# Performance work log

Hardware: AMD Instinct MI355X
Metric: run time of the kernel (lower is better)

The kernel has to match this reference:

```python
import jax, jax.numpy as jnp
import numpy as np

N_NODES = 100000
N_EDGES = 1600000
IN_DIM = 128
HID = 128


def sage_conv(x, src, dst, W_l, W_r, b, num_nodes):
    # PyG SAGEConv (mean aggregation): out = lin_l(mean_{j in N(i)} x_j) + lin_r(x_i)
    msgs = x[src]                                            # [E, F] gather
    agg = jax.ops.segment_sum(msgs, dst, num_segments=num_nodes)  # [N, F]
    cnt = jax.ops.segment_sum(jnp.ones((src.shape[0],), x.dtype), dst,
                              num_segments=num_nodes)        # [N]
    agg = agg / jnp.maximum(cnt, 1.0)[:, None]               # mean; 0 for isolated nodes
    return agg @ W_l + b + x @ W_r


def setup_inputs() -> dict:
    key = jax.random.key(0)
    ks = jax.random.split(key, 12)
    s_in = 1.0 / np.sqrt(IN_DIM)
    s_h = 1.0 / np.sqrt(HID)
    return {
        "x": jax.random.normal(ks[0], (N_NODES, IN_DIM), jnp.float32),
        "edge_index": jax.random.randint(ks[1], (2, N_EDGES), 0, N_NODES, jnp.int64),
        "Wl1": jax.random.normal(ks[2], (IN_DIM, HID), jnp.float32) * s_in,
        "Wr1": jax.random.normal(ks[3], (IN_DIM, HID), jnp.float32) * s_in,
        "b1": jnp.zeros((HID,), jnp.float32),
        "Wl2": jax.random.normal(ks[4], (HID, HID), jnp.float32) * s_h,
        "Wr2": jax.random.normal(ks[5], (HID, HID), jnp.float32) * s_h,
        "b2": jnp.zeros((HID,), jnp.float32),
        "Wp": jax.random.normal(ks[6], (HID, 1), jnp.float32) * s_h,
        "bp": jnp.zeros((1,), jnp.float32),
        "Wd": jax.random.normal(ks[7], (HID, 1), jnp.float32) * s_h,
        "bd": jnp.zeros((1,), jnp.float32),
    }


def reference(x, edge_index, Wl1, Wr1, b1, Wl2, Wr2, b2, Wp, bp, Wd, bd):
    src, dst = edge_index[0], edge_index[1]
    h = jax.nn.relu(sage_conv(x, src, dst, Wl1, Wr1, b1, N_NODES))
    h = jax.nn.relu(sage_conv(h, src, dst, Wl2, Wr2, b2, N_NODES))
    preds = h @ Wp + bp                      # [N, 1]
    diffs = jax.nn.sigmoid(h @ Wd + bd)      # [N, 1]
    return (preds - diffs, preds + diffs)
```

## Files before the change

### kernel.cpp

```cpp
#include <hip/hip_runtime.h>
#include <hip/hip_bf16.h>

#define N_NODES 100000
#define N_EDGES 1600000
#define NBUCK 1563
#define BCAP 1216
#define PADC 1408
#define ACHUNK 4096
#define GTILES 1563
#define PABLK 391

typedef __bf16 bf16x8 __attribute__((ext_vector_type(8)));
typedef __bf16 bf16x4 __attribute__((ext_vector_type(4)));
typedef float  f32x4  __attribute__((ext_vector_type(4)));
typedef float  f32x2  __attribute__((ext_vector_type(2)));


#define ACC16(v)                                             \
  a01 += __builtin_amdgcn_cvt_pk_f32_fp8((v).x, false);      \
  a23 += __builtin_amdgcn_cvt_pk_f32_fp8((v).x, true);       \
  a45 += __builtin_amdgcn_cvt_pk_f32_fp8((v).y, false);      \
  a67 += __builtin_amdgcn_cvt_pk_f32_fp8((v).y, true);       \
  a89 += __builtin_amdgcn_cvt_pk_f32_fp8((v).z, false);      \
  aAB += __builtin_amdgcn_cvt_pk_f32_fp8((v).z, true);       \
  aCD += __builtin_amdgcn_cvt_pk_f32_fp8((v).w, false);      \
  aEF += __builtin_amdgcn_cvt_pk_f32_fp8((v).w, true);

#define WFRAG(ct, c) (*(const bf16x8*)&Wswz[(size_t)((((w * 4 + (ct)) * 4 + (c)) * 64) + lane) * 8])


__global__ __launch_bounds__(256) void init_kernel(int* __restrict__ bcnt,
                                                   int* __restrict__ P1s,
                                                   int* __restrict__ P2s,
                                                   const float* __restrict__ Wl1,
                                                   const float* __restrict__ Wr1,
                                                   const float* __restrict__ Wl2,
                                                   const float* __restrict__ Wr2,
                                                   __bf16* __restrict__ W1out,
                                                   __bf16* __restrict__ W2out) {
  const int b = blockIdx.x, t = threadIdx.x;
  if (b == 0) {
    for (int i = t; i < NBUCK; i += 256) bcnt[i] = 0;
    if (t < 32) { P1s[t] = 0; P2s[t] = 0; }
    return;
  }
  int gi = (b - 1) * 256 + t;
  bool L2 = gi >= 32768;
  int i = gi & 32767;
  int j = i & 7;
  int lane = (i >> 3) & 63;
  int c = (i >> 9) & 3;
  int tile = i >> 11;
  int k = c * 32 + ((lane >> 4) * 8) + j;
  int krow = L2 ? (((k & 7) << 4) | (k >> 3)) : k;
  int col = tile * 16 + (lane & 15);
  const float* Wl = L2 ? Wl2 : Wl1;
  const float* Wr = L2 ? Wr2 : Wr1;
  float v = (col < 128) ? Wl[krow * 128 + col] : Wr[krow * 128 + (col - 128)];
  (L2 ? W2out : W1out)[i] = (__bf16)v;
}


__global__ __launch_bounds__(256, 4) void work1_kernel(
    const float* __restrict__ A, const __bf16* __restrict__ Wswz,
    const float* __restrict__ bias, unsigned char* __restrict__ P,
    __bf16* __restrict__ R, int M,
    const int* __restrict__ src, const int* __restrict__ dst,
    int* __restrict__ bcnt, unsigned* __restrict__ packed, int E) {
  __shared__ __align__(16) char smem[64 * 144 * 2];
  const int t = threadIdx.x;

  if (blockIdx.x < PABLK) {
    int* hist = (int*)smem;
    int* curs = (int*)(smem + 6272);
    for (int i = t; i < NBUCK; i += 256) hist[i] = 0;
    __syncthreads();

    const int base = blockIdx.x * ACHUNK;
    const int lim = min(base + ACHUNK, E);

    int dloc[16], sloc[16];
    int myn = 0;
    for (int i = base + t; i < lim; i += 256) {
      dloc[myn] = dst[i];
      sloc[myn] = src[i];
      ++myn;
    }
    for (int k = 0; k < myn; ++k) atomicAdd(&hist[dloc[k] >> 6], 1);
    __syncthreads();

    for (int i = t; i < NBUCK; i += 256) {
      int h = hist[i];
      curs[i] = (h > 0) ? atomicAdd(&bcnt[i], h) : 0;
    }
    __syncthreads();

    for (int k = 0; k < myn; ++k) {
      int d = dloc[k];
      int b = d >> 6;
      int pos = atomicAdd(&curs[b], 1);
      if (pos < BCAP)
        packed[(size_t)b * BCAP + pos] = ((unsigned)sloc[k] << 6) | (unsigned)(d & 63);
    }
    return;
  }

  __bf16 (*ldsA)[144] = (__bf16 (*)[144])smem;
  const int lane = t & 63;
  const int w = t >> 6;
  const int q = lane >> 4;
  const int s = lane & 15;
  const int m0 = (blockIdx.x - PABLK) * 64;

#pragma unroll
  for (int it = 0; it < 8; ++it) {
    int row = it * 8 + (t >> 5);
    int col = (t & 31) * 4;
    float4 v = make_float4(0.f, 0.f, 0.f, 0.f);
    if (m0 + row < M) v = *(const float4*)&A[(size_t)(m0 + row) * 128 + col];
    bf16x4 bv;
    bv.x = (__bf16)v.x; bv.y = (__bf16)v.y; bv.z = (__bf16)v.z; bv.w = (__bf16)v.w;
    *(bf16x4*)&ldsA[row][col] = bv;
  }

  float breg[4];
#pragma unroll
  for (int j = 0; j < 4; ++j)
    breg[j] = (w >= 2) ? bias[((w - 2) * 4 + j) * 16 + s] : 0.f;

  __syncthreads();

#pragma unroll
  for (int half = 0; half < 2; ++half) {
    f32x4 acc[8];
    f32x4 zero = {0.f, 0.f, 0.f, 0.f};
#pragma unroll
    for (int i = 0; i < 8; ++i) acc[i] = zero;

    bf16x8 b0 = WFRAG(0, 0), b1 = WFRAG(1, 0), b2 = WFRAG(2, 0), b3 = WFRAG(3, 0);
#pragma unroll
    for (int c = 0; c < 4; ++c) {
      bf16x8 n0, n1, n2, n3;
      if (c < 3) { n0 = WFRAG(0, c + 1); n1 = WFRAG(1, c + 1); n2 = WFRAG(2, c + 1); n3 = WFRAG(3, c + 1); }
      bf16x8 a0 = *(const bf16x8*)&ldsA[(half * 2 + 0) * 16 + s][c * 32 + q * 8];
      bf16x8 a1 = *(const bf16x8*)&ldsA[(half * 2 + 1) * 16 + s][c * 32 + q * 8];
      acc[0] = __builtin_amdgcn_mfma_f32_16x16x32_bf16(a0, b0, acc[0], 0, 0, 0);
      acc[4] = __builtin_amdgcn_mfma_f32_16x16x32_bf16(a1, b0, acc[4], 0, 0, 0);
      acc[1] = __builtin_amdgcn_mfma_f32_16x16x32_bf16(a0, b1, acc[1], 0, 0, 0);
      acc[5] = __builtin_amdgcn_mfma_f32_16x16x32_bf16(a1, b1, acc[5], 0, 0, 0);
      acc[2] = __builtin_amdgcn_mfma_f32_16x16x32_bf16(a0, b2, acc[2], 0, 0, 0);
      acc[6] = __builtin_amdgcn_mfma_f32_16x16x32_bf16(a1, b2, acc[6], 0, 0, 0);
      acc[3] = __builtin_amdgcn_mfma_f32_16x16x32_bf16(a0, b3, acc[3], 0, 0, 0);
      acc[7] = __builtin_amdgcn_mfma_f32_16x16x32_bf16(a1, b3, acc[7], 0, 0, 0);
      if (c < 3) { b0 = n0; b1 = n1; b2 = n2; b3 = n3; }
    }

#pragma unroll
    for (int i = 0; i < 2; ++i) {
      int rt = half * 2 + i;
#pragma unroll
      for (int r = 0; r < 4; ++r) {
        int row = m0 + rt * 16 + q * 4 + r;
        if (row < M) {
          if (w < 2) {
            unsigned v = 0;
            v = __builtin_amdgcn_cvt_pk_fp8_f32(acc[i * 4 + 0][r], acc[i * 4 + 1][r], v, false);
            v = __builtin_amdgcn_cvt_pk_fp8_f32(acc[i * 4 + 2][r], acc[i * 4 + 3][r], v, true);
            *(unsigned*)&P[(size_t)row * 128 + s * 8 + w * 4] = v;
          } else {
            bf16x4 o;
#pragma unroll
            for (int ct = 0; ct < 4; ++ct) o[ct] = (__bf16)(acc[i * 4 + ct][r] + breg[ct]);
            *(bf16x4*)&R[(size_t)row * 128 + s * 8 + (w - 2) * 4] = o;
          }
        }
      }
    }
  }
}


__global__ __launch_bounds__(256, 4) void fusedB_kernel(
    const unsigned char* __restrict__ P1, __bf16* R,
    const unsigned* __restrict__ pck, const int* __restrict__ bcnt,
    const __bf16* __restrict__ Wswz, const float* __restrict__ bias,
    unsigned char* __restrict__ P2, int* __restrict__ srt,
    int* __restrict__ meta, int N) {
  __shared__ __bf16 Hlds[64][144];
  __shared__ int ssrcL[PADC];
  __shared__ int hist[64], pexcl[64], curs[64], scanb[64];
  __shared__ int gsteal;
  const int t = threadIdx.x;
  const int lane = t & 63;
  const int w = t >> 6;
  const int q = lane >> 4;
  const int s = lane & 15;
  const int b = blockIdx.x, nb = b * 64;

  if (t < 64) hist[t] = 0;
  if (t == 0) gsteal = 0;
  __syncthreads();

  const int ecnt = min(bcnt[b], BCAP);
  const unsigned* pk = pck + (size_t)b * BCAP;
  unsigned ploc[5];
  int myn = 0;
  for (int i = t; i < ecnt; i += 256) {
    unsigned p = pk[i];
    ploc[myn++] = p;
    atomicAdd(&hist[p & 63u], 1);
  }
  __syncthreads();

  int c0 = (t < 64) ? hist[t] : 0;
  int pc = (c0 + 3) & ~3;
  int x = pc;
  if (t < 64) scanb[t] = x;
  __syncthreads();
  for (int d = 1; d < 64; d <<= 1) {
    int y = (t >= d && t < 64) ? scanb[t - d] : 0;
    __syncthreads();
    if (t < 64) { x += y; scanb[t] = x; }
    __syncthreads();
  }
  if (t < 64) { pexcl[t] = x - pc; curs[t] = x - pc; }
  __syncthreads();

  for (int k = 0; k < myn; ++k) {
    unsigned p = ploc[k];
    int r = atomicAdd(&curs[p & 63u], 1);
    ssrcL[r] = (int)(p >> 6);
  }
  if (t < 64)
    for (int j = c0; j < pc; ++j) ssrcL[pexcl[t] + j] = N;
  __syncthreads();

  for (int i = t; i < PADC; i += 256) srt[(size_t)b * PADC + i] = ssrcL[i];
  if (t < 64) meta[b * 64 + t] = (pexcl[t] << 16) | hist[t];

  const int s8 = lane & 7;
  const int g8 = lane >> 3;
  const unsigned char* Pb = P1 + (size_t)s8 * 16;
  for (;;) {
    int n8;
    if (lane == 0) n8 = atomicAdd(&gsteal, 8);
    n8 = __shfl(n8, 0, 64);
    if (n8 >= 64) break;
    int dl = n8 + g8;
    int node = nb + dl;
    int start = pexcl[dl];
    int dg = hist[dl];
    int pend = start + ((dg + 3) & ~3);

    f32x2 a01 = {0.f, 0.f}, a23 = {0.f, 0.f}, a45 = {0.f, 0.f}, a67 = {0.f, 0.f};
    f32x2 a89 = {0.f, 0.f}, aAB = {0.f, 0.f}, aCD = {0.f, 0.f}, aEF = {0.f, 0.f};
    int cur = start;
    for (; cur + 8 <= pend; cur += 8) {
      int4 sv0 = *(const int4*)&ssrcL[cur];
      int4 sv1 = *(const int4*)&ssrcL[cur + 4];
      uint4 v0 = *(const uint4*)(Pb + (size_t)sv0.x * 128);
      uint4 v1 = *(const uint4*)(Pb + (size_t)sv0.y * 128);
      uint4 v2 = *(const uint4*)(Pb + (size_t)sv0.z * 128);
      uint4 v3 = *(const uint4*)(Pb + (size_t)sv0.w * 128);
      uint4 v4 = *(const uint4*)(Pb + (size_t)sv1.x * 128);
      uint4 v5 = *(const uint4*)(Pb + (size_t)sv1.y * 128);
      uint4 v6 = *(const uint4*)(Pb + (size_t)sv1.z * 128);
      uint4 v7 = *(const uint4*)(Pb + (size_t)sv1.w * 128);
      ACC16(v0) ACC16(v1) ACC16(v2) ACC16(v3)
      ACC16(v4) ACC16(v5) ACC16(v6) ACC16(v7)
    }
    if (cur < pend) {
      int4 sv = *(const int4*)&ssrcL[cur];
      uint4 v0 = *(const uint4*)(Pb + (size_t)sv.x * 128);
      uint4 v1 = *(const uint4*)(Pb + (size_t)sv.y * 128);
      uint4 v2 = *(const uint4*)(Pb + (size_t)sv.z * 128);
      uint4 v3 = *(const uint4*)(Pb + (size_t)sv.w * 128);
      ACC16(v0) ACC16(v1) ACC16(v2) ACC16(v3)
    }

    int nc = min(node, N - 1);
    float inv = 1.0f / (float)(dg > 0 ? dg : 1);
    const int p16 = s8 * 16;
    bf16x8 rv0 = *(const bf16x8*)&R[(size_t)nc * 128 + p16];
    bf16x8 rv1 = *(const bf16x8*)&R[(size_t)nc * 128 + p16 + 8];
    float ac[16] = {a01[0], a01[1], a23[0], a23[1], a45[0], a45[1], a67[0], a67[1],
                    a89[0], a89[1], aAB[0], aAB[1], aCD[0], aCD[1], aEF[0], aEF[1]};
    bf16x8 h0, h1;
#pragma unroll
    for (int j = 0; j < 8; ++j) {
      h0[j] = (__bf16)fmaxf(ac[j] * inv + (float)rv0[j], 0.f);
      h1[j] = (__bf16)fmaxf(ac[8 + j] * inv + (float)rv1[j], 0.f);
    }
    *(bf16x8*)&Hlds[dl][p16] = h0;
    *(bf16x8*)&Hlds[dl][p16 + 8] = h1;
  }
  __syncthreads();

  float breg[4];
#pragma unroll
  for (int j = 0; j < 4; ++j)
    breg[j] = (w >= 2) ? bias[((w - 2) * 4 + j) * 16 + s] : 0.f;

#pragma unroll
  for (int half = 0; half < 2; ++half) {
    f32x4 acc[8];
    f32x4 zero = {0.f, 0.f, 0.f, 0.f};
#pragma unroll
    for (int i = 0; i < 8; ++i) acc[i] = zero;

#pragma unroll
    for (int c = 0; c < 4; ++c) {
      bf16x8 a0 = *(const bf16x8*)&Hlds[(half * 2 + 0) * 16 + s][c * 32 + q * 8];
      bf16x8 a1 = *(const bf16x8*)&Hlds[(half * 2 + 1) * 16 + s][c * 32 + q * 8];
#pragma unroll
      for (int ct = 0; ct < 4; ++ct) {
        bf16x8 b = *(const bf16x8*)&Wswz[(size_t)((((w * 4 + ct) * 4 + c) * 64) + lane) * 8];
        acc[ct]     = __builtin_amdgcn_mfma_f32_16x16x32_bf16(a0, b, acc[ct], 0, 0, 0);
        acc[4 + ct] = __builtin_amdgcn_mfma_f32_16x16x32_bf16(a1, b, acc[4 + ct], 0, 0, 0);
      }
    }

#pragma unroll
    for (int i = 0; i < 2; ++i) {
      int rt = half * 2 + i;
#pragma unroll
      for (int r = 0; r < 4; ++r) {
        int row = nb + rt * 16 + q * 4 + r;
        if (row < N) {
          if (w < 2) {
            unsigned v = 0;
            v = __builtin_amdgcn_cvt_pk_fp8_f32(acc[i * 4 + 0][r], acc[i * 4 + 1][r], v, false);
            v = __builtin_amdgcn_cvt_pk_fp8_f32(acc[i * 4 + 2][r], acc[i * 4 + 3][r], v, true);
            *(unsigned*)&P2[(size_t)row * 128 + s * 8 + w * 4] = v;
          } else {
            bf16x4 o;
#pragma unroll
            for (int ct = 0; ct < 4; ++ct) o[ct] = (__bf16)(acc[i * 4 + ct][r] + breg[ct]);
            *(bf16x4*)&R[(size_t)row * 128 + s * 8 + (w - 2) * 4] = o;
          }
        }
      }
    }
  }
}


__global__ __launch_bounds__(256, 4) void fusedC_kernel(
    const unsigned char* __restrict__ P2, const __bf16* __restrict__ R,
    const int* __restrict__ srt, const int* __restrict__ meta,
    float* __restrict__ out,
    const float* __restrict__ Wp, const float* __restrict__ Wd,
    const float* __restrict__ bp, const float* __restrict__ bd, int N) {
  __shared__ int ssrcL[PADC];
  __shared__ int hist[64], pexcl[64];
  __shared__ int gsteal;
  const int t = threadIdx.x;
  const int lane = t & 63;
  const int b = blockIdx.x, nb = b * 64;

  for (int i = t; i < PADC; i += 256) ssrcL[i] = srt[(size_t)b * PADC + i];
  if (t < 64) {
    int m = meta[b * 64 + t];
    pexcl[t] = m >> 16;
    hist[t] = m & 0xffff;
  }
  if (t == 0) gsteal = 0;
  __syncthreads();

  const int s8 = lane & 7;
  const int g8 = lane >> 3;
  const unsigned char* Pb = P2 + (size_t)s8 * 16;
  for (;;) {
    int n8;
    if (lane == 0) n8 = atomicAdd(&gsteal, 8);
    n8 = __shfl(n8, 0, 64);
    if (n8 >= 64) break;
    int dl = n8 + g8;
    int node = nb + dl;
    int start = pexcl[dl];
    int dg = hist[dl];
    int pend = start + ((dg + 3) & ~3);

    f32x2 a01 = {0.f, 0.f}, a23 = {0.f, 0.f}, a45 = {0.f, 0.f}, a67 = {0.f, 0.f};
    f32x2 a89 = {0.f, 0.f}, aAB = {0.f, 0.f}, aCD = {0.f, 0.f}, aEF = {0.f, 0.f};
    int cur = start;
    for (; cur + 8 <= pend; cur += 8) {
      int4 sv0 = *(const int4*)&ssrcL[cur];
      int4 sv1 = *(const int4*)&ssrcL[cur + 4];
      uint4 v0 = *(const uint4*)(Pb + (size_t)sv0.x * 128);
      uint4 v1 = *(const uint4*)(Pb + (size_t)sv0.y * 128);
      uint4 v2 = *(const uint4*)(Pb + (size_t)sv0.z * 128);
      uint4 v3 = *(const uint4*)(Pb + (size_t)sv0.w * 128);
      uint4 v4 = *(const uint4*)(Pb + (size_t)sv1.x * 128);
      uint4 v5 = *(const uint4*)(Pb + (size_t)sv1.y * 128);
      uint4 v6 = *(const uint4*)(Pb + (size_t)sv1.z * 128);
      uint4 v7 = *(const uint4*)(Pb + (size_t)sv1.w * 128);
      ACC16(v0) ACC16(v1) ACC16(v2) ACC16(v3)
      ACC16(v4) ACC16(v5) ACC16(v6) ACC16(v7)
    }
    if (cur < pend) {
      int4 sv = *(const int4*)&ssrcL[cur];
      uint4 v0 = *(const uint4*)(Pb + (size_t)sv.x * 128);
      uint4 v1 = *(const uint4*)(Pb + (size_t)sv.y * 128);
      uint4 v2 = *(const uint4*)(Pb + (size_t)sv.z * 128);
      uint4 v3 = *(const uint4*)(Pb + (size_t)sv.w * 128);
      ACC16(v0) ACC16(v1) ACC16(v2) ACC16(v3)
    }

    int nc = min(node, N - 1);
    float inv = 1.0f / (float)(dg > 0 ? dg : 1);
    const int p16 = s8 * 16;
    bf16x8 rv0 = *(const bf16x8*)&R[(size_t)nc * 128 + p16];
    bf16x8 rv1 = *(const bf16x8*)&R[(size_t)nc * 128 + p16 + 8];
    float ac[16] = {a01[0], a01[1], a23[0], a23[1], a45[0], a45[1], a67[0], a67[1],
                    a89[0], a89[1], aAB[0], aAB[1], aCD[0], aCD[1], aEF[0], aEF[1]};
    float p = 0.f, dd = 0.f;
#pragma unroll
    for (int j = 0; j < 16; ++j) {
      int pos = p16 + j;
      int f = ((pos & 7) << 4) | (pos >> 3);
      float rvj = (float)((j < 8) ? rv0[j] : rv1[j - 8]);
      float h = fmaxf(ac[j] * inv + rvj, 0.f);
      p += h * Wp[f];
      dd += h * Wd[f];
    }
    p += __shfl_xor(p, 1, 64);  p += __shfl_xor(p, 2, 64);  p += __shfl_xor(p, 4, 64);
    dd += __shfl_xor(dd, 1, 64); dd += __shfl_xor(dd, 2, 64); dd += __shfl_xor(dd, 4, 64);
    if (node < N && s8 == 0) {
      float preds = p + bp[0];
      float sg = 1.0f / (1.0f + __expf(-(dd + bd[0])));
      out[node] = preds - sg;
      out[N + node] = preds + sg;
    }
  }
}


extern "C" void kernel_launch(void* const* d_in, const int* in_sizes, int n_in,
                              void* d_out, int out_size, void* d_ws, size_t ws_size,
                              hipStream_t stream) {
  const float* x    = (const float*)d_in[0];
  const int*   ei   = (const int*)d_in[1];
  const float* Wl1 = (const float*)d_in[2];
  const float* Wr1 = (const float*)d_in[3];
  const float* b1  = (const float*)d_in[4];
  const float* Wl2 = (const float*)d_in[5];
  const float* Wr2 = (const float*)d_in[6];
  const float* b2  = (const float*)d_in[7];
  const float* Wp  = (const float*)d_in[8];
  const float* bp  = (const float*)d_in[9];
  const float* Wd  = (const float*)d_in[10];
  const float* bd  = (const float*)d_in[11];
  float* out = (float*)d_out;

  const int N = N_NODES, E = N_EDGES;
  const int* src = ei;
  const int* dst = ei + E;

  char* w = (char*)d_ws;
  unsigned char* P1 = (unsigned char*)w; w += (size_t)(N + 1) * 128;
  unsigned char* P2 = (unsigned char*)w; w += (size_t)(N + 1) * 128;
  __bf16* Rbuf   = (__bf16*)w;   w += (size_t)N * 128 * 2;
  unsigned* pck  = (unsigned*)w; w += (size_t)NBUCK * BCAP * 4;
  int* bcnt      = (int*)w;      w += (size_t)(NBUCK + 32) * 4;
  __bf16* Ws1    = (__bf16*)w;   w += 65536;
  __bf16* Ws2    = (__bf16*)w;   w += 65536;
  int* srt       = (int*)w;      w += (size_t)NBUCK * PADC * 4;
  int* meta      = (int*)w;      w += (size_t)NBUCK * 64 * 4;

  init_kernel<<<257, 256, 0, stream>>>(bcnt,
                                       (int*)(P1 + (size_t)N * 128),
                                       (int*)(P2 + (size_t)N * 128),
                                       Wl1, Wr1, Wl2, Wr2, Ws1, Ws2);
  work1_kernel<<<GTILES + PABLK, 256, 0, stream>>>(x, Ws1, b1, P1, Rbuf, N,
                                                   src, dst, bcnt, pck, E);
  fusedB_kernel<<<NBUCK, 256, 0, stream>>>(P1, Rbuf, pck, bcnt, Ws2, b2, P2,
                                           srt, meta, N);
  fusedC_kernel<<<NBUCK, 256, 0, stream>>>(P2, Rbuf, srt, meta, out,
                                           Wp, Wd, bp, bd, N);
}
```

Measured before the change: 230.1 us.

## Enlarge partition chunks, drop register staging and prefetch, raise fusedC occupancy

Edge partition blocks now each handle 16384 edges (98 blocks instead of 391), and src/dst are re-read from global memory rather than staged in register arrays. The W-fragment software prefetch in the GEMM loop is removed in favour of in-loop loads, and the 8-wide gather unroll in fusedC is collapsed to a 4-wide loop with launch bounds raised to 6 waves per SIMD. The aim is to cut register pressure and raise occupancy. The cost is less memory-level parallelism per wave, fewer partition blocks, and a second global read of the edge arrays.

```diff
diff --git a/kernel.cpp b/kernel.cpp
--- a/kernel.cpp
+++ b/kernel.cpp
@@ -6,9 +6,9 @@
 #define NBUCK 1563
 #define BCAP 1216
 #define PADC 1408
-#define ACHUNK 4096
+#define ACHUNK 16384
 #define GTILES 1563
-#define PABLK 391
+#define PABLK 98
 
 typedef __bf16 bf16x8 __attribute__((ext_vector_type(8)));
 typedef __bf16 bf16x4 __attribute__((ext_vector_type(4)));
@@ -25,8 +25,6 @@
   aAB += __builtin_amdgcn_cvt_pk_f32_fp8((v).z, true);       \
   aCD += __builtin_amdgcn_cvt_pk_f32_fp8((v).w, false);      \
   aEF += __builtin_amdgcn_cvt_pk_f32_fp8((v).w, true);
-
-#define WFRAG(ct, c) (*(const bf16x8*)&Wswz[(size_t)((((w * 4 + (ct)) * 4 + (c)) * 64) + lane) * 8])
 
 
 __global__ __launch_bounds__(256) void init_kernel(int* __restrict__ bcnt,
@@ -79,14 +77,8 @@
     const int base = blockIdx.x * ACHUNK;
     const int lim = min(base + ACHUNK, E);
 
-    int dloc[16], sloc[16];
-    int myn = 0;
-    for (int i = base + t; i < lim; i += 256) {
-      dloc[myn] = dst[i];
-      sloc[myn] = src[i];
-      ++myn;
-    }
-    for (int k = 0; k < myn; ++k) atomicAdd(&hist[dloc[k] >> 6], 1);
+    for (int i = base + t; i < lim; i += 256)
+      atomicAdd(&hist[dst[i] >> 6], 1);
     __syncthreads();
 
     for (int i = t; i < NBUCK; i += 256) {
@@ -95,12 +87,12 @@
     }
     __syncthreads();
 
-    for (int k = 0; k < myn; ++k) {
-      int d = dloc[k];
+    for (int i = base + t; i < lim; i += 256) {
+      int d = dst[i];
       int b = d >> 6;
       int pos = atomicAdd(&curs[b], 1);
       if (pos < BCAP)
-        packed[(size_t)b * BCAP + pos] = ((unsigned)sloc[k] << 6) | (unsigned)(d & 63);
+        packed[(size_t)b * BCAP + pos] = ((unsigned)src[i] << 6) | (unsigned)(d & 63);
     }
     return;
   }
@@ -137,22 +129,16 @@
 #pragma unroll
     for (int i = 0; i < 8; ++i) acc[i] = zero;
 
-    bf16x8 b0 = WFRAG(0, 0), b1 = WFRAG(1, 0), b2 = WFRAG(2, 0), b3 = WFRAG(3, 0);
 #pragma unroll
     for (int c = 0; c < 4; ++c) {
-      bf16x8 n0, n1, n2, n3;
-      if (c < 3) { n0 = WFRAG(0, c + 1); n1 = WFRAG(1, c + 1); n2 = WFRAG(2, c + 1); n3 = WFRAG(3, c + 1); }
       bf16x8 a0 = *(const bf16x8*)&ldsA[(half * 2 + 0) * 16 + s][c * 32 + q * 8];
       bf16x8 a1 = *(const bf16x8*)&ldsA[(half * 2 + 1) * 16 + s][c * 32 + q * 8];
-      acc[0] = __builtin_amdgcn_mfma_f32_16x16x32_bf16(a0, b0, acc[0], 0, 0, 0);
-      acc[4] = __builtin_amdgcn_mfma_f32_16x16x32_bf16(a1, b0, acc[4], 0, 0, 0);
-      acc[1] = __builtin_amdgcn_mfma_f32_16x16x32_bf16(a0, b1, acc[1], 0, 0, 0);
-      acc[5] = __builtin_amdgcn_mfma_f32_16x16x32_bf16(a1, b1, acc[5], 0, 0, 0);
-      acc[2] = __builtin_amdgcn_mfma_f32_16x16x32_bf16(a0, b2, acc[2], 0, 0, 0);
-      acc[6] = __builtin_amdgcn_mfma_f32_16x16x32_bf16(a1, b2, acc[6], 0, 0, 0);
-      acc[3] = __builtin_amdgcn_mfma_f32_16x16x32_bf16(a0, b3, acc[3], 0, 0, 0);
-      acc[7] = __builtin_amdgcn_mfma_f32_16x16x32_bf16(a1, b3, acc[7], 0, 0, 0);
-      if (c < 3) { b0 = n0; b1 = n1; b2 = n2; b3 = n3; }
+#pragma unroll
+      for (int ct = 0; ct < 4; ++ct) {
+        bf16x8 b = *(const bf16x8*)&Wswz[(size_t)((((w * 4 + ct) * 4 + c) * 64) + lane) * 8];
+        acc[ct]     = __builtin_amdgcn_mfma_f32_16x16x32_bf16(a0, b, acc[ct], 0, 0, 0);
+        acc[4 + ct] = __builtin_amdgcn_mfma_f32_16x16x32_bf16(a1, b, acc[4 + ct], 0, 0, 0);
+      }
     }
 
 #pragma unroll
@@ -345,7 +331,7 @@
 }
 
 
-__global__ __launch_bounds__(256, 4) void fusedC_kernel(
+__global__ __launch_bounds__(256, 6) void fusedC_kernel(
     const unsigned char* __restrict__ P2, const __bf16* __restrict__ R,
     const int* __restrict__ srt, const int* __restrict__ meta,
     float* __restrict__ out,
@@ -383,22 +369,7 @@
 
     f32x2 a01 = {0.f, 0.f}, a23 = {0.f, 0.f}, a45 = {0.f, 0.f}, a67 = {0.f, 0.f};
     f32x2 a89 = {0.f, 0.f}, aAB = {0.f, 0.f}, aCD = {0.f, 0.f}, aEF = {0.f, 0.f};
-    int cur = start;
-    for (; cur + 8 <= pend; cur += 8) {
-      int4 sv0 = *(const int4*)&ssrcL[cur];
-      int4 sv1 = *(const int4*)&ssrcL[cur + 4];
-      uint4 v0 = *(const uint4*)(Pb + (size_t)sv0.x * 128);
-      uint4 v1 = *(const uint4*)(Pb + (size_t)sv0.y * 128);
-      uint4 v2 = *(const uint4*)(Pb + (size_t)sv0.z * 128);
-      uint4 v3 = *(const uint4*)(Pb + (size_t)sv0.w * 128);
-      uint4 v4 = *(const uint4*)(Pb + (size_t)sv1.x * 128);
-      uint4 v5 = *(const uint4*)(Pb + (size_t)sv1.y * 128);
-      uint4 v6 = *(const uint4*)(Pb + (size_t)sv1.z * 128);
-      uint4 v7 = *(const uint4*)(Pb + (size_t)sv1.w * 128);
-      ACC16(v0) ACC16(v1) ACC16(v2) ACC16(v3)
-      ACC16(v4) ACC16(v5) ACC16(v6) ACC16(v7)
-    }
-    if (cur < pend) {
+    for (int cur = start; cur < pend; cur += 4) {
       int4 sv = *(const int4*)&ssrcL[cur];
       uint4 v0 = *(const uint4*)(Pb + (size_t)sv.x * 128);
       uint4 v1 = *(const uint4*)(Pb + (size_t)sv.y * 128);
```

New measurement: 264.5 us. 1.15x slower.
